# Optimization experiments

Hardware: AMD Instinct MI355X
Metric: run time of the kernel (lower is better)

## Reference

```python
import jax, jax.numpy as jnp
import numpy as np

B, N, E0, F_IN, H, EMB, VEC, DPI = 1024, 256, 2048, 6, 32, 32, 26, 512


def setup_inputs() -> dict:
    key = jax.random.key(0)
    ks = jax.random.split(key, 16)
    # fixed urban scene graph, shared by every batch element, with self-loops
    src0 = jax.random.randint(ks[0], (E0,), 0, N, dtype=jnp.int32)
    dst0 = jax.random.randint(ks[1], (E0,), 0, N, dtype=jnp.int32)
    loops = jnp.arange(N, dtype=jnp.int32)
    src = jnp.concatenate([src0, loops])
    dst = jnp.concatenate([dst0, loops])

    s = 0.05
    return {
        "graph_feats": jax.random.normal(ks[2], (B, N, F_IN), jnp.float32),
        "vector": jax.random.normal(ks[3], (B, VEC), jnp.float32),
        "src": src,
        "dst": dst,
        "W1": jax.random.normal(ks[4], (F_IN, H), jnp.float32) * s,
        "b1": jnp.zeros((H,), jnp.float32),
        "W2": jax.random.normal(ks[5], (H, H), jnp.float32) * s,
        "b2": jnp.zeros((H,), jnp.float32),
        "W3": jax.random.normal(ks[6], (H, H), jnp.float32) * s,
        "b3": jnp.zeros((H,), jnp.float32),
        "W_emb": jax.random.normal(ks[7], (H, EMB), jnp.float32) * s,
        "b_emb": jnp.zeros((EMB,), jnp.float32),
        "W_pi": jax.random.normal(ks[8], (VEC + EMB, DPI), jnp.float32) * s,
        "b_pi": jnp.zeros((DPI,), jnp.float32),
        "W_vf": jax.random.normal(ks[9], (VEC + EMB, DPI), jnp.float32) * s,
        "b_vf": jnp.zeros((DPI,), jnp.float32),
    }


def _edge_norm(src, dst, n_nodes):
    # DGL GraphConv norm='both': out_deg(src)^-1/2 * in_deg(dst)^-1/2
    ones = jnp.ones(src.shape[0], jnp.float32)
    deg_out = jax.ops.segment_sum(ones, src, num_segments=n_nodes)
    deg_in = jax.ops.segment_sum(ones, dst, num_segments=n_nodes)
    inv_o = jnp.where(deg_out > 0, deg_out ** -0.5, 0.0)
    inv_i = jnp.where(deg_in > 0, deg_in ** -0.5, 0.0)
    return inv_o[src] * inv_i[dst]  # [E]


def _gconv(h, src, dst, norm, W, b):
    # h: [B, N, F]; symmetric-normalized aggregation then linear (DGL GraphConv)
    msg = h[:, src, :] * norm[None, :, None]          # [B, E, F]
    agg = jnp.zeros_like(h).at[:, dst, :].add(msg)     # [B, N, F]
    return agg @ W + b


def reference(graph_feats, vector, src, dst, W1, b1, W2, b2, W3, b3,
              W_emb, b_emb, W_pi, b_pi, W_vf, b_vf):
    n_nodes = graph_feats.shape[1]
    norm = _edge_norm(src, dst, n_nodes)
    h = jax.nn.relu(_gconv(graph_feats, src, dst, norm, W1, b1))
    h = jax.nn.relu(_gconv(h, src, dst, norm, W2, b2))
    h = jax.nn.relu(_gconv(h, src, dst, norm, W3, b3))  # three_layers=True
    hg = jnp.mean(h, axis=1)                 # dgl.mean_nodes -> [B, H]
    emb = hg @ W_emb + b_emb                 # [B, EMB]
    comb = jnp.concatenate([vector[:, :26], emb], axis=1)  # [B, 58]
    pi = jax.nn.relu(comb @ W_pi + b_pi)
    vf = jax.nn.relu(comb @ W_vf + b_vf)
    return pi, vf
```

## Files before the change

### kernel.cpp

```cpp
#include <hip/hip_runtime.h>

#define B_    1024
#define N_    256
#define E_    2304
#define FIN_  6
#define VEC_  26
#define STR_  36

#define WS_ROWPTR   0
#define WS_PACKED   1088
#define WS_PERM     19520

__global__ __launch_bounds__(256) void prep_kernel(
    const int* __restrict__ src, const int* __restrict__ dst,
    char* __restrict__ ws)
{
    __shared__ int   deg_o[N_], deg_i[N_];
    __shared__ float inv_o[N_], inv_i[N_];
    __shared__ int   scan[N_];
    __shared__ int   rp[N_ + 1];
    __shared__ int   cursor[N_];
    __shared__ int   bcnt[64], boff[64];

    int*  row_ptr_g = (int*)(ws + WS_ROWPTR);
    int2* packed_g  = (int2*)(ws + WS_PACKED);
    int*  perm_g    = (int*)(ws + WS_PERM);

    const int t = threadIdx.x;

    deg_o[t] = 0; deg_i[t] = 0;
    if (t < 64) bcnt[t] = 0;
    __syncthreads();

    for (int e = t; e < E_; e += 256) {
        atomicAdd(&deg_o[src[e]], 1);
        atomicAdd(&deg_i[dst[e]], 1);
    }
    __syncthreads();
    {
        int dO = deg_o[t], dI = deg_i[t];
        inv_o[t] = dO > 0 ? rsqrtf((float)dO) : 0.f;
        inv_i[t] = dI > 0 ? rsqrtf((float)dI) : 0.f;
        scan[t] = dI;
    }
    __syncthreads();
    for (int off = 1; off < N_; off <<= 1) {
        int v = (t >= off) ? scan[t - off] : 0;
        __syncthreads();
        scan[t] += v;
        __syncthreads();
    }
    rp[t + 1] = scan[t];
    if (t == 0) rp[0] = 0;
    __syncthreads();
    cursor[t]    = rp[t];
    row_ptr_g[t] = rp[t];
    if (t == 0) row_ptr_g[N_] = rp[N_];
    __syncthreads();
    for (int e = t; e < E_; e += 256) {
        int d = dst[e], s = src[e];
        int pos = atomicAdd(&cursor[d], 1);
        packed_g[pos] = make_int2(s, __float_as_int(inv_o[s] * inv_i[d]));
    }

    int dmy = deg_i[t]; if (dmy > 63) dmy = 63;
    atomicAdd(&bcnt[dmy], 1);
    __syncthreads();
    if (t == 0) { int run = 0; for (int i = 0; i < 64; ++i) { boff[i] = run; run += bcnt[i]; } }
    __syncthreads();
    { int pos = atomicAdd(&boff[dmy], 1); perm_g[pos] = t; }
}

__global__ __launch_bounds__(256) void main_kernel(
    const float* __restrict__ gf,
    const float* __restrict__ vec,
    const float* __restrict__ W1, const float* __restrict__ b1,
    const float* __restrict__ W2, const float* __restrict__ b2,
    const float* __restrict__ W3, const float* __restrict__ b3,
    const float* __restrict__ We, const float* __restrict__ be,
    const float* __restrict__ Wpi, const float* __restrict__ bpi,
    const float* __restrict__ Wvf, const float* __restrict__ bvf,
    const char* __restrict__ ws,
    float2* __restrict__ out)
{
    __shared__ __align__(16) float buf[N_ * STR_];
    __shared__ float part[8 * 33];
    __shared__ float hgl[32];
    __shared__ float comb[VEC_ + 32];

    const int t = threadIdx.x;
    const int b = blockIdx.x;

    const int*  row_ptr = (const int*)(ws + WS_ROWPTR);
    const int2* packed  = (const int2*)(ws + WS_PACKED);
    const int   node    = ((const int*)(ws + WS_PERM))[t];

    {
        const float* g = gf + (size_t)b * (N_ * FIN_);
        for (int i = t; i < N_ * 8; i += 256) {
            int n = i >> 3, k = i & 7;
            buf[n * STR_ + k] = (k < FIN_) ? g[n * FIN_ + k] : 0.f;
        }
    }
    const int beg = row_ptr[node], end = row_ptr[node + 1];
    __syncthreads();

    float o[32];

    {
        float a[8] = {0,0,0,0,0,0,0,0};
        for (int e = beg; e < end; ++e) {
            int2 p = packed[e];
            float w = __int_as_float(p.y);
            const float4* hr = (const float4*)&buf[p.x * STR_];
            float4 c0 = hr[0], c1 = hr[1];
            a[0] += w * c0.x; a[1] += w * c0.y; a[2] += w * c0.z; a[3] += w * c0.w;
            a[4] += w * c1.x; a[5] += w * c1.y;
        }
#pragma unroll
        for (int j = 0; j < 32; ++j) o[j] = b1[j];
#pragma unroll
        for (int k = 0; k < FIN_; ++k) {
            float ak = a[k];
            const float* wr = &W1[k * 32];
#pragma unroll
            for (int j = 0; j < 32; ++j) o[j] += ak * wr[j];
        }
#pragma unroll
        for (int j = 0; j < 32; ++j) o[j] = fmaxf(o[j], 0.f);
    }
    __syncthreads();
    {
        float4* row = (float4*)&buf[node * STR_];
#pragma unroll
        for (int q = 0; q < 8; ++q) row[q] = make_float4(o[4*q], o[4*q+1], o[4*q+2], o[4*q+3]);
    }
    __syncthreads();

    for (int L = 0; L < 2; ++L) {
        float acc[32];
#pragma unroll
        for (int k = 0; k < 32; ++k) acc[k] = 0.f;
        for (int e = beg; e < end; ++e) {
            int2 p = packed[e];
            float w = __int_as_float(p.y);
            const float4* hr = (const float4*)&buf[p.x * STR_];
#pragma unroll
            for (int q = 0; q < 8; ++q) {
                float4 c = hr[q];
                acc[4*q]   += w * c.x;
                acc[4*q+1] += w * c.y;
                acc[4*q+2] += w * c.z;
                acc[4*q+3] += w * c.w;
            }
        }
        const float* Wl = (L == 0) ? W2 : W3;
        const float* Bl = (L == 0) ? b2 : b3;
#pragma unroll
        for (int j = 0; j < 32; ++j) o[j] = Bl[j];
#pragma unroll 8
        for (int k = 0; k < 32; ++k) {
            float ak = acc[k];
            const float* wr = &Wl[k * 32];
#pragma unroll
            for (int j = 0; j < 32; ++j) o[j] += ak * wr[j];
        }
#pragma unroll
        for (int j = 0; j < 32; ++j) o[j] = fmaxf(o[j], 0.f);
        __syncthreads();
        {
            float4* row = (float4*)&buf[node * STR_];
#pragma unroll
            for (int q = 0; q < 8; ++q) row[q] = make_float4(o[4*q], o[4*q+1], o[4*q+2], o[4*q+3]);
        }
        __syncthreads();
    }

    {
        int j = t & 31, g = t >> 5;
        float s = 0.f;
        for (int i = 0; i < 32; ++i) s += buf[(g * 32 + i) * STR_ + j];
        part[g * 33 + j] = s;
    }
    __syncthreads();
    if (t < 32) {
        float sum = 0.f;
#pragma unroll
        for (int g = 0; g < 8; ++g) sum += part[g * 33 + t];
        hgl[t] = sum * (1.0f / 256.0f);
    }
    __syncthreads();

    if (t < 32) {
        float v = be[t];
#pragma unroll
        for (int j = 0; j < 32; ++j) v += hgl[j] * We[j * 32 + t];
        comb[VEC_ + t] = v;
    }
    if (t < VEC_) comb[t] = vec[b * VEC_ + t];
    __syncthreads();

    {
        float p0 = bpi[2 * t], p1 = bpi[2 * t + 1];
        float v0 = bvf[2 * t], v1 = bvf[2 * t + 1];
        const float2* Wp = (const float2*)Wpi;
        const float2* Wv = (const float2*)Wvf;
        for (int k = 0; k < VEC_ + 32; ++k) {
            float c = comb[k];
            float2 a = Wp[k * 256 + t];
            p0 += c * a.x; p1 += c * a.y;
            float2 d = Wv[k * 256 + t];
            v0 += c * d.x; v1 += c * d.y;
        }
        out[b * 256 + t]          = make_float2(fmaxf(p0, 0.f), fmaxf(p1, 0.f));
        out[262144 + b * 256 + t] = make_float2(fmaxf(v0, 0.f), fmaxf(v1, 0.f));
    }
}

extern "C" void kernel_launch(void* const* d_in, const int* in_sizes, int n_in,
                              void* d_out, int out_size, void* d_ws, size_t ws_size,
                              hipStream_t stream)
{
    prep_kernel<<<1, 256, 0, stream>>>(
        (const int*)d_in[2], (const int*)d_in[3], (char*)d_ws);
    main_kernel<<<B_, 256, 0, stream>>>(
        (const float*)d_in[0], (const float*)d_in[1],
        (const float*)d_in[4], (const float*)d_in[5],
        (const float*)d_in[6], (const float*)d_in[7],
        (const float*)d_in[8], (const float*)d_in[9],
        (const float*)d_in[10], (const float*)d_in[11],
        (const float*)d_in[12], (const float*)d_in[13],
        (const float*)d_in[14], (const float*)d_in[15],
        (const char*)d_ws, (float2*)d_out);
}
```

Baseline: 138.4 us.

## Fuse graph CSR preprocessing into main kernel with fp16-packed edges in LDS

```diff
diff --git a/kernel.cpp b/kernel.cpp
--- a/kernel.cpp
+++ b/kernel.cpp
@@ -1,89 +1,28 @@
 #include <hip/hip_runtime.h>
+#include <hip/hip_fp16.h>
 
 #define B_    1024
 #define N_    256
 #define E_    2304
+#define EPT_  9
 #define FIN_  6
 #define VEC_  26
 #define STR_  36
 
-#define WS_ROWPTR   0
-#define WS_PACKED   1088
-#define WS_PERM     19520
-
-__global__ __launch_bounds__(256) void prep_kernel(
-    const int* __restrict__ src, const int* __restrict__ dst,
-    char* __restrict__ ws)
-{
-    __shared__ int   deg_o[N_], deg_i[N_];
-    __shared__ float inv_o[N_], inv_i[N_];
-    __shared__ int   scan[N_];
-    __shared__ int   rp[N_ + 1];
-    __shared__ int   cursor[N_];
-    __shared__ int   bcnt[64], boff[64];
-
-    int*  row_ptr_g = (int*)(ws + WS_ROWPTR);
-    int2* packed_g  = (int2*)(ws + WS_PACKED);
-    int*  perm_g    = (int*)(ws + WS_PERM);
-
-    const int t = threadIdx.x;
-
-    deg_o[t] = 0; deg_i[t] = 0;
-    if (t < 64) bcnt[t] = 0;
-    __syncthreads();
-
-    for (int e = t; e < E_; e += 256) {
-        atomicAdd(&deg_o[src[e]], 1);
-        atomicAdd(&deg_i[dst[e]], 1);
-    }
-    __syncthreads();
-    {
-        int dO = deg_o[t], dI = deg_i[t];
-        inv_o[t] = dO > 0 ? rsqrtf((float)dO) : 0.f;
-        inv_i[t] = dI > 0 ? rsqrtf((float)dI) : 0.f;
-        scan[t] = dI;
-    }
-    __syncthreads();
-    for (int off = 1; off < N_; off <<= 1) {
-        int v = (t >= off) ? scan[t - off] : 0;
-        __syncthreads();
-        scan[t] += v;
-        __syncthreads();
-    }
-    rp[t + 1] = scan[t];
-    if (t == 0) rp[0] = 0;
-    __syncthreads();
-    cursor[t]    = rp[t];
-    row_ptr_g[t] = rp[t];
-    if (t == 0) row_ptr_g[N_] = rp[N_];
-    __syncthreads();
-    for (int e = t; e < E_; e += 256) {
-        int d = dst[e], s = src[e];
-        int pos = atomicAdd(&cursor[d], 1);
-        packed_g[pos] = make_int2(s, __float_as_int(inv_o[s] * inv_i[d]));
-    }
-
-    int dmy = deg_i[t]; if (dmy > 63) dmy = 63;
-    atomicAdd(&bcnt[dmy], 1);
-    __syncthreads();
-    if (t == 0) { int run = 0; for (int i = 0; i < 64; ++i) { boff[i] = run; run += bcnt[i]; } }
-    __syncthreads();
-    { int pos = atomicAdd(&boff[dmy], 1); perm_g[pos] = t; }
-}
-
-__global__ __launch_bounds__(256) void main_kernel(
+__global__ __launch_bounds__(256) void fused_kernel(
     const float* __restrict__ gf,
     const float* __restrict__ vec,
+    const int* __restrict__ src, const int* __restrict__ dst,
     const float* __restrict__ W1, const float* __restrict__ b1,
     const float* __restrict__ W2, const float* __restrict__ b2,
     const float* __restrict__ W3, const float* __restrict__ b3,
     const float* __restrict__ We, const float* __restrict__ be,
     const float* __restrict__ Wpi, const float* __restrict__ bpi,
     const float* __restrict__ Wvf, const float* __restrict__ bvf,
-    const char* __restrict__ ws,
     float2* __restrict__ out)
 {
     __shared__ __align__(16) float buf[N_ * STR_];
+    __shared__ unsigned int packedE[E_];
     __shared__ float part[8 * 33];
     __shared__ float hgl[32];
     __shared__ float comb[VEC_ + 32];
@@ -91,9 +30,68 @@
     const int t = threadIdx.x;
     const int b = blockIdx.x;
 
-    const int*  row_ptr = (const int*)(ws + WS_ROWPTR);
-    const int2* packed  = (const int2*)(ws + WS_PACKED);
-    const int   node    = ((const int*)(ws + WS_PERM))[t];
+    int*   deg_o  = (int*)buf;
+    int*   deg_i  = (int*)buf + 256;
+    int*   scan   = (int*)buf + 512;
+    int*   cursor = (int*)buf + 768;
+    int*   bcnt   = (int*)buf + 1024;
+    int*   boff   = (int*)buf + 1088;
+    int*   perm   = (int*)buf + 1152;
+    float* inv_o  = buf + 1408;
+    float* inv_i  = buf + 1664;
+
+    deg_o[t] = 0; deg_i[t] = 0;
+    if (t < 64) bcnt[t] = 0;
+    __syncthreads();
+
+    int sB[EPT_], dB[EPT_];
+#pragma unroll
+    for (int i = 0; i < EPT_; ++i) {
+        int e = t + 256 * i;
+        sB[i] = src[e]; dB[i] = dst[e];
+    }
+#pragma unroll
+    for (int i = 0; i < EPT_; ++i) {
+        atomicAdd(&deg_o[sB[i]], 1);
+        atomicAdd(&deg_i[dB[i]], 1);
+    }
+    __syncthreads();
+
+    const int dI = deg_i[t];
+    {
+        int dO = deg_o[t];
+        inv_o[t] = dO > 0 ? rsqrtf((float)dO) : 0.f;
+        inv_i[t] = dI > 0 ? rsqrtf((float)dI) : 0.f;
+        scan[t] = dI;
+    }
+    __syncthreads();
+    for (int off = 1; off < N_; off <<= 1) {
+        int v = (t >= off) ? scan[t - off] : 0;
+        __syncthreads();
+        scan[t] += v;
+        __syncthreads();
+    }
+    cursor[t] = scan[t] - dI;
+    int dmy = dI > 63 ? 63 : dI;
+    atomicAdd(&bcnt[dmy], 1);
+    __syncthreads();
+    if (t == 0) { int run = 0; for (int i = 0; i < 64; ++i) { boff[i] = run; run += bcnt[i]; } }
+    __syncthreads();
+    { int pos = atomicAdd(&boff[dmy], 1); perm[pos] = t; }
+#pragma unroll
+    for (int i = 0; i < EPT_; ++i) {
+        int s = sB[i], d = dB[i];
+        int pos = atomicAdd(&cursor[d], 1);
+        float nrm = inv_o[s] * inv_i[d];
+        unsigned short h = __half_as_ushort(__float2half(nrm));
+        packedE[pos] = ((unsigned int)s << 16) | (unsigned int)h;
+    }
+    __syncthreads();
+
+    const int node = perm[t];
+    const int end  = scan[node];
+    const int beg  = end - deg_i[node];
+    __syncthreads();
 
     {
         const float* g = gf + (size_t)b * (N_ * FIN_);
@@ -102,7 +100,6 @@
             buf[n * STR_ + k] = (k < FIN_) ? g[n * FIN_ + k] : 0.f;
         }
     }
-    const int beg = row_ptr[node], end = row_ptr[node + 1];
     __syncthreads();
 
     float o[32];
@@ -110,9 +107,9 @@
     {
         float a[8] = {0,0,0,0,0,0,0,0};
         for (int e = beg; e < end; ++e) {
-            int2 p = packed[e];
-            float w = __int_as_float(p.y);
-            const float4* hr = (const float4*)&buf[p.x * STR_];
+            unsigned int u = packedE[e];
+            float w = __half2float(__ushort_as_half((unsigned short)(u & 0xffffu)));
+            const float4* hr = (const float4*)&buf[(u >> 16) * STR_];
             float4 c0 = hr[0], c1 = hr[1];
             a[0] += w * c0.x; a[1] += w * c0.y; a[2] += w * c0.z; a[3] += w * c0.w;
             a[4] += w * c1.x; a[5] += w * c1.y;
@@ -142,9 +139,9 @@
 #pragma unroll
         for (int k = 0; k < 32; ++k) acc[k] = 0.f;
         for (int e = beg; e < end; ++e) {
-            int2 p = packed[e];
-            float w = __int_as_float(p.y);
-            const float4* hr = (const float4*)&buf[p.x * STR_];
+            unsigned int u = packedE[e];
+            float w = __half2float(__ushort_as_half((unsigned short)(u & 0xffffu)));
+            const float4* hr = (const float4*)&buf[(u >> 16) * STR_];
 #pragma unroll
             for (int q = 0; q < 8; ++q) {
                 float4 c = hr[q];
@@ -221,15 +218,14 @@
                               void* d_out, int out_size, void* d_ws, size_t ws_size,
                               hipStream_t stream)
 {
-    prep_kernel<<<1, 256, 0, stream>>>(
-        (const int*)d_in[2], (const int*)d_in[3], (char*)d_ws);
-    main_kernel<<<B_, 256, 0, stream>>>(
+    fused_kernel<<<B_, 256, 0, stream>>>(
         (const float*)d_in[0], (const float*)d_in[1],
+        (const int*)d_in[2], (const int*)d_in[3],
         (const float*)d_in[4], (const float*)d_in[5],
         (const float*)d_in[6], (const float*)d_in[7],
         (const float*)d_in[8], (const float*)d_in[9],
         (const float*)d_in[10], (const float*)d_in[11],
         (const float*)d_in[12], (const float*)d_in[13],
         (const float*)d_in[14], (const float*)d_in[15],
-        (const char*)d_ws, (float2*)d_out);
+        (float2*)d_out);
 }
```

New measurement: 139.9 us. No clear change (+1.1%).

## Run GCN layers in packed fp16 with compressed edges staged in LDS

Applied to the files above, without the earlier changes.

```diff
diff --git a/kernel.cpp b/kernel.cpp
--- a/kernel.cpp
+++ b/kernel.cpp
@@ -1,18 +1,37 @@
 #include <hip/hip_runtime.h>
+#include <hip/hip_fp16.h>
 
 #define B_    1024
 #define N_    256
 #define E_    2304
 #define FIN_  6
 #define VEC_  26
-#define STR_  36
-
-#define WS_ROWPTR   0
-#define WS_PACKED   1088
-#define WS_PERM     19520
+#define HSTR_ 40
+
+#define WS_ROWPTR 0
+#define WS_PACKED 1088
+#define WS_PERM   10304
+#define WS_WH     11328
+#define OH_W1 0
+#define OH_W2 192
+#define OH_W3 1216
+#define OH_B1 2240
+#define OH_B2 2272
+#define OH_B3 2304
+
+__device__ __forceinline__ __half2 relu2(__half2 x) {
+    union { __half2 h; unsigned int u; } v;
+    v.h = x;
+    unsigned int mask = ((v.u & 0x80008000u) >> 15) * 0xFFFFu;
+    v.u &= ~mask;
+    return v.h;
+}
 
 __global__ __launch_bounds__(256) void prep_kernel(
     const int* __restrict__ src, const int* __restrict__ dst,
+    const float* __restrict__ W1, const float* __restrict__ b1,
+    const float* __restrict__ W2, const float* __restrict__ b2,
+    const float* __restrict__ W3, const float* __restrict__ b3,
     char* __restrict__ ws)
 {
     __shared__ int   deg_o[N_], deg_i[N_];
@@ -22,9 +41,10 @@
     __shared__ int   cursor[N_];
     __shared__ int   bcnt[64], boff[64];
 
-    int*  row_ptr_g = (int*)(ws + WS_ROWPTR);
-    int2* packed_g  = (int2*)(ws + WS_PACKED);
-    int*  perm_g    = (int*)(ws + WS_PERM);
+    int*          row_ptr_g = (int*)(ws + WS_ROWPTR);
+    unsigned int* packed_g  = (unsigned int*)(ws + WS_PACKED);
+    int*          perm_g    = (int*)(ws + WS_PERM);
+    __half*       Wh        = (__half*)(ws + WS_WH);
 
     const int t = threadIdx.x;
 
@@ -60,7 +80,9 @@
     for (int e = t; e < E_; e += 256) {
         int d = dst[e], s = src[e];
         int pos = atomicAdd(&cursor[d], 1);
-        packed_g[pos] = make_int2(s, __float_as_int(inv_o[s] * inv_i[d]));
+        float nrm = inv_o[s] * inv_i[d];
+        unsigned short h = __half_as_ushort(__float2half(nrm));
+        packed_g[pos] = ((unsigned int)s << 16) | (unsigned int)h;
     }
 
     int dmy = deg_i[t]; if (dmy > 63) dmy = 63;
@@ -69,21 +91,28 @@
     if (t == 0) { int run = 0; for (int i = 0; i < 64; ++i) { boff[i] = run; run += bcnt[i]; } }
     __syncthreads();
     { int pos = atomicAdd(&boff[dmy], 1); perm_g[pos] = t; }
+
+    for (int i = t; i < 192;  i += 256) Wh[OH_W1 + i] = __float2half(W1[i]);
+    for (int i = t; i < 1024; i += 256) Wh[OH_W2 + i] = __float2half(W2[i]);
+    for (int i = t; i < 1024; i += 256) Wh[OH_W3 + i] = __float2half(W3[i]);
+    if (t < 32) {
+        Wh[OH_B1 + t] = __float2half(b1[t]);
+        Wh[OH_B2 + t] = __float2half(b2[t]);
+        Wh[OH_B3 + t] = __float2half(b3[t]);
+    }
 }
 
 __global__ __launch_bounds__(256) void main_kernel(
     const float* __restrict__ gf,
     const float* __restrict__ vec,
-    const float* __restrict__ W1, const float* __restrict__ b1,
-    const float* __restrict__ W2, const float* __restrict__ b2,
-    const float* __restrict__ W3, const float* __restrict__ b3,
     const float* __restrict__ We, const float* __restrict__ be,
     const float* __restrict__ Wpi, const float* __restrict__ bpi,
     const float* __restrict__ Wvf, const float* __restrict__ bvf,
     const char* __restrict__ ws,
     float2* __restrict__ out)
 {
-    __shared__ __align__(16) float buf[N_ * STR_];
+    __shared__ __align__(16) __half hbuf[N_ * HSTR_];
+    __shared__ unsigned int packedE[E_];
     __shared__ float part[8 * 33];
     __shared__ float hgl[32];
     __shared__ float comb[VEC_ + 32];
@@ -91,102 +120,122 @@
     const int t = threadIdx.x;
     const int b = blockIdx.x;
 
-    const int*  row_ptr = (const int*)(ws + WS_ROWPTR);
-    const int2* packed  = (const int2*)(ws + WS_PACKED);
-    const int   node    = ((const int*)(ws + WS_PERM))[t];
+    const int*          row_ptr = (const int*)(ws + WS_ROWPTR);
+    const unsigned int* packedG = (const unsigned int*)(ws + WS_PACKED);
+    const int           node    = ((const int*)(ws + WS_PERM))[t];
+    const __half*       Wh      = (const __half*)(ws + WS_WH);
+
+    const int beg = row_ptr[node], end = row_ptr[node + 1];
+
+    for (int e = t; e < E_; e += 256) packedE[e] = packedG[e];
 
     {
         const float* g = gf + (size_t)b * (N_ * FIN_);
         for (int i = t; i < N_ * 8; i += 256) {
             int n = i >> 3, k = i & 7;
-            buf[n * STR_ + k] = (k < FIN_) ? g[n * FIN_ + k] : 0.f;
-        }
-    }
-    const int beg = row_ptr[node], end = row_ptr[node + 1];
-    __syncthreads();
-
-    float o[32];
-
-    {
-        float a[8] = {0,0,0,0,0,0,0,0};
+            hbuf[n * HSTR_ + k] = __float2half((k < FIN_) ? g[n * FIN_ + k] : 0.f);
+        }
+    }
+    __syncthreads();
+
+    const __half2 z2 = __float2half2_rn(0.f);
+    __half2 o2[16];
+
+    {
+        __half2 a2[4] = {z2, z2, z2, z2};
         for (int e = beg; e < end; ++e) {
-            int2 p = packed[e];
-            float w = __int_as_float(p.y);
-            const float4* hr = (const float4*)&buf[p.x * STR_];
-            float4 c0 = hr[0], c1 = hr[1];
-            a[0] += w * c0.x; a[1] += w * c0.y; a[2] += w * c0.z; a[3] += w * c0.w;
-            a[4] += w * c1.x; a[5] += w * c1.y;
-        }
-#pragma unroll
-        for (int j = 0; j < 32; ++j) o[j] = b1[j];
+            unsigned int u = packedE[e];
+            __half2 w2 = __half2half2(__ushort_as_half((unsigned short)(u & 0xffffu)));
+            union { float4 f4; __half2 h2[4]; } r;
+            r.f4 = *(const float4*)&hbuf[(u >> 16) * HSTR_];
+#pragma unroll
+            for (int q = 0; q < 4; ++q) a2[q] = __hfma2(w2, r.h2[q], a2[q]);
+        }
+        const __half2* bh = (const __half2*)(Wh + OH_B1);
+#pragma unroll
+        for (int j = 0; j < 16; ++j) o2[j] = bh[j];
 #pragma unroll
         for (int k = 0; k < FIN_; ++k) {
-            float ak = a[k];
-            const float* wr = &W1[k * 32];
-#pragma unroll
-            for (int j = 0; j < 32; ++j) o[j] += ak * wr[j];
-        }
-#pragma unroll
-        for (int j = 0; j < 32; ++j) o[j] = fmaxf(o[j], 0.f);
-    }
-    __syncthreads();
-    {
-        float4* row = (float4*)&buf[node * STR_];
-#pragma unroll
-        for (int q = 0; q < 8; ++q) row[q] = make_float4(o[4*q], o[4*q+1], o[4*q+2], o[4*q+3]);
+            __half ak = (k & 1) ? __high2half(a2[k >> 1]) : __low2half(a2[k >> 1]);
+            __half2 ak2 = __half2half2(ak);
+            const __half2* wr = (const __half2*)(Wh + OH_W1 + k * 32);
+#pragma unroll
+            for (int j = 0; j < 16; ++j) o2[j] = __hfma2(ak2, wr[j], o2[j]);
+        }
+#pragma unroll
+        for (int j = 0; j < 16; ++j) o2[j] = relu2(o2[j]);
+    }
+    __syncthreads();
+    {
+        union { float4 f4; __half2 h2[4]; } w;
+        float4* row = (float4*)&hbuf[node * HSTR_];
+#pragma unroll
+        for (int q = 0; q < 4; ++q) {
+#pragma unroll
+            for (int r = 0; r < 4; ++r) w.h2[r] = o2[4 * q + r];
+            row[q] = w.f4;
+        }
     }
     __syncthreads();
 
     for (int L = 0; L < 2; ++L) {
-        float acc[32];
-#pragma unroll
-        for (int k = 0; k < 32; ++k) acc[k] = 0.f;
+        __half2 acc2[16];
+#pragma unroll
+        for (int j = 0; j < 16; ++j) acc2[j] = z2;
         for (int e = beg; e < end; ++e) {
-            int2 p = packed[e];
-            float w = __int_as_float(p.y);
-            const float4* hr = (const float4*)&buf[p.x * STR_];
-#pragma unroll
-            for (int q = 0; q < 8; ++q) {
-                float4 c = hr[q];
-                acc[4*q]   += w * c.x;
-                acc[4*q+1] += w * c.y;
-                acc[4*q+2] += w * c.z;
-                acc[4*q+3] += w * c.w;
+            unsigned int u = packedE[e];
+            __half2 w2 = __half2half2(__ushort_as_half((unsigned short)(u & 0xffffu)));
+            const float4* hr = (const float4*)&hbuf[(u >> 16) * HSTR_];
+            union { float4 f4; __half2 h2[4]; } r0, r1, r2, r3;
+            r0.f4 = hr[0]; r1.f4 = hr[1]; r2.f4 = hr[2]; r3.f4 = hr[3];
+#pragma unroll
+            for (int q = 0; q < 4; ++q) {
+                acc2[q]      = __hfma2(w2, r0.h2[q], acc2[q]);
+                acc2[4 + q]  = __hfma2(w2, r1.h2[q], acc2[4 + q]);
+                acc2[8 + q]  = __hfma2(w2, r2.h2[q], acc2[8 + q]);
+                acc2[12 + q] = __hfma2(w2, r3.h2[q], acc2[12 + q]);
             }
         }
-        const float* Wl = (L == 0) ? W2 : W3;
-        const float* Bl = (L == 0) ? b2 : b3;
-#pragma unroll
-        for (int j = 0; j < 32; ++j) o[j] = Bl[j];
+        const __half*  Whl = Wh + (L == 0 ? OH_W2 : OH_W3);
+        const __half2* bh  = (const __half2*)(Wh + (L == 0 ? OH_B2 : OH_B3));
+#pragma unroll
+        for (int j = 0; j < 16; ++j) o2[j] = bh[j];
 #pragma unroll 8
         for (int k = 0; k < 32; ++k) {
-            float ak = acc[k];
-            const float* wr = &Wl[k * 32];
-#pragma unroll
-            for (int j = 0; j < 32; ++j) o[j] += ak * wr[j];
-        }
-#pragma unroll
-        for (int j = 0; j < 32; ++j) o[j] = fmaxf(o[j], 0.f);
+            __half ak = (k & 1) ? __high2half(acc2[k >> 1]) : __low2half(acc2[k >> 1]);
+            __half2 ak2 = __half2half2(ak);
+            const __half2* wr = (const __half2*)(Whl + k * 32);
+#pragma unroll
+            for (int j = 0; j < 16; ++j) o2[j] = __hfma2(ak2, wr[j], o2[j]);
+        }
+#pragma unroll
+        for (int j = 0; j < 16; ++j) o2[j] = relu2(o2[j]);
         __syncthreads();
         {
-            float4* row = (float4*)&buf[node * STR_];
-#pragma unroll
-            for (int q = 0; q < 8; ++q) row[q] = make_float4(o[4*q], o[4*q+1], o[4*q+2], o[4*q+3]);
-        }
-        __syncthreads();
-    }
-
-    {
-        int j = t & 31, g = t >> 5;
+            union { float4 f4; __half2 h2[4]; } w;
+            float4* row = (float4*)&hbuf[node * HSTR_];
+#pragma unroll
+            for (int q = 0; q < 4; ++q) {
+#pragma unroll
+                for (int r = 0; r < 4; ++r) w.h2[r] = o2[4 * q + r];
+                row[q] = w.f4;
+            }
+        }
+        __syncthreads();
+    }
+
+    {
+        int j = t & 31, g8 = t >> 5;
         float s = 0.f;
-        for (int i = 0; i < 32; ++i) s += buf[(g * 32 + i) * STR_ + j];
-        part[g * 33 + j] = s;
+        for (int i = 0; i < 32; ++i)
+            s += __half2float(hbuf[(g8 * 32 + i) * HSTR_ + j]);
+        part[g8 * 33 + j] = s;
     }
     __syncthreads();
     if (t < 32) {
         float sum = 0.f;
 #pragma unroll
-        for (int g = 0; g < 8; ++g) sum += part[g * 33 + t];
+        for (int g8 = 0; g8 < 8; ++g8) sum += part[g8 * 33 + t];
         hgl[t] = sum * (1.0f / 256.0f);
     }
     __syncthreads();
@@ -222,12 +271,13 @@
                               hipStream_t stream)
 {
     prep_kernel<<<1, 256, 0, stream>>>(
-        (const int*)d_in[2], (const int*)d_in[3], (char*)d_ws);
-    main_kernel<<<B_, 256, 0, stream>>>(
-        (const float*)d_in[0], (const float*)d_in[1],
+        (const int*)d_in[2], (const int*)d_in[3],
         (const float*)d_in[4], (const float*)d_in[5],
         (const float*)d_in[6], (const float*)d_in[7],
         (const float*)d_in[8], (const float*)d_in[9],
+        (char*)d_ws);
+    main_kernel<<<B_, 256, 0, stream>>>(
+        (const float*)d_in[0], (const float*)d_in[1],
         (const float*)d_in[10], (const float*)d_in[11],
         (const float*)d_in[12], (const float*)d_in[13],
         (const float*)d_in[14], (const float*)d_in[15],
```

New measurement: 138.3 us. Within noise of the previous version (-0.1%).

## Replace sparse gather aggregation with dense fp16 adjacency MFMA matmuls

Applied to the files above, without the earlier changes.

```diff
diff --git a/kernel.cpp b/kernel.cpp
--- a/kernel.cpp
+++ b/kernel.cpp
@@ -1,37 +1,33 @@
 #include <hip/hip_runtime.h>
+#include <hip/hip_fp16.h>
 
 #define B_    1024
 #define N_    256
 #define E_    2304
 #define FIN_  6
 #define VEC_  26
-#define STR_  36
-
-#define WS_ROWPTR   0
-#define WS_PACKED   1088
-#define WS_PERM     19520
+#define HSTR_ 40
+#define ZSTR_ 264
+#define NT_   512
+
+typedef _Float16 half8 __attribute__((ext_vector_type(8)));
+typedef float    f32x4 __attribute__((ext_vector_type(4)));
+
 
 __global__ __launch_bounds__(256) void prep_kernel(
     const int* __restrict__ src, const int* __restrict__ dst,
     char* __restrict__ ws)
 {
-    __shared__ int   deg_o[N_], deg_i[N_];
+    __shared__ int   deg_o[N_], deg_i[N_], scan[N_], rp[N_ + 1], cursor[N_];
     __shared__ float inv_o[N_], inv_i[N_];
-    __shared__ int   scan[N_];
-    __shared__ int   rp[N_ + 1];
-    __shared__ int   cursor[N_];
-    __shared__ int   bcnt[64], boff[64];
-
-    int*  row_ptr_g = (int*)(ws + WS_ROWPTR);
-    int2* packed_g  = (int2*)(ws + WS_PACKED);
-    int*  perm_g    = (int*)(ws + WS_PERM);
+    __shared__ unsigned int packedE[E_];
 
     const int t = threadIdx.x;
+    __half*       A   = (__half*)ws;
+    unsigned int* A32 = (unsigned int*)ws;
 
     deg_o[t] = 0; deg_i[t] = 0;
-    if (t < 64) bcnt[t] = 0;
-    __syncthreads();
-
+    __syncthreads();
     for (int e = t; e < E_; e += 256) {
         atomicAdd(&deg_o[src[e]], 1);
         atomicAdd(&deg_i[dst[e]], 1);
@@ -53,25 +49,27 @@
     rp[t + 1] = scan[t];
     if (t == 0) rp[0] = 0;
     __syncthreads();
-    cursor[t]    = rp[t];
-    row_ptr_g[t] = rp[t];
-    if (t == 0) row_ptr_g[N_] = rp[N_];
+    cursor[t] = rp[t];
     __syncthreads();
     for (int e = t; e < E_; e += 256) {
         int d = dst[e], s = src[e];
         int pos = atomicAdd(&cursor[d], 1);
-        packed_g[pos] = make_int2(s, __float_as_int(inv_o[s] * inv_i[d]));
-    }
-
-    int dmy = deg_i[t]; if (dmy > 63) dmy = 63;
-    atomicAdd(&bcnt[dmy], 1);
-    __syncthreads();
-    if (t == 0) { int run = 0; for (int i = 0; i < 64; ++i) { boff[i] = run; run += bcnt[i]; } }
-    __syncthreads();
-    { int pos = atomicAdd(&boff[dmy], 1); perm_g[pos] = t; }
+        float nrm = inv_o[s] * inv_i[d];
+        packedE[pos] = ((unsigned int)s << 16)
+                     | (unsigned int)__half_as_ushort(__float2half(nrm));
+    }
+    for (int i = t; i < 32768; i += 256) A32[i] = 0u;
+    __syncthreads();
+    for (int e = rp[t]; e < rp[t + 1]; ++e) {
+        unsigned int u = packedE[e];
+        int s = (int)(u >> 16);
+        float nv = __half2float(__ushort_as_half((unsigned short)(u & 0xffffu)));
+        __half* p = &A[t * 256 + s];
+        *p = __float2half(__half2float(*p) + nv);
+    }
 }
 
-__global__ __launch_bounds__(256) void main_kernel(
+__global__ __launch_bounds__(512) void main_kernel(
     const float* __restrict__ gf,
     const float* __restrict__ vec,
     const float* __restrict__ W1, const float* __restrict__ b1,
@@ -81,112 +79,136 @@
     const float* __restrict__ Wpi, const float* __restrict__ bpi,
     const float* __restrict__ Wvf, const float* __restrict__ bvf,
     const char* __restrict__ ws,
-    float2* __restrict__ out)
+    float* __restrict__ out)
 {
-    __shared__ __align__(16) float buf[N_ * STR_];
-    __shared__ float part[8 * 33];
+    __shared__ __align__(16) __half hbuf[N_ * HSTR_];
+    __shared__ __align__(16) __half zT[32 * ZSTR_];
+    __shared__ float part[16 * 33];
     __shared__ float hgl[32];
     __shared__ float comb[VEC_ + 32];
 
     const int t = threadIdx.x;
     const int b = blockIdx.x;
-
-    const int*  row_ptr = (const int*)(ws + WS_ROWPTR);
-    const int2* packed  = (const int2*)(ws + WS_PACKED);
-    const int   node    = ((const int*)(ws + WS_PERM))[t];
-
-    {
-        const float* g = gf + (size_t)b * (N_ * FIN_);
-        for (int i = t; i < N_ * 8; i += 256) {
-            int n = i >> 3, k = i & 7;
-            buf[n * STR_ + k] = (k < FIN_) ? g[n * FIN_ + k] : 0.f;
-        }
-    }
-    const int beg = row_ptr[node], end = row_ptr[node + 1];
-    __syncthreads();
-
-    float o[32];
-
-    {
-        float a[8] = {0,0,0,0,0,0,0,0};
-        for (int e = beg; e < end; ++e) {
-            int2 p = packed[e];
-            float w = __int_as_float(p.y);
-            const float4* hr = (const float4*)&buf[p.x * STR_];
-            float4 c0 = hr[0], c1 = hr[1];
-            a[0] += w * c0.x; a[1] += w * c0.y; a[2] += w * c0.z; a[3] += w * c0.w;
-            a[4] += w * c1.x; a[5] += w * c1.y;
-        }
-#pragma unroll
-        for (int j = 0; j < 32; ++j) o[j] = b1[j];
-#pragma unroll
-        for (int k = 0; k < FIN_; ++k) {
-            float ak = a[k];
-            const float* wr = &W1[k * 32];
-#pragma unroll
-            for (int j = 0; j < 32; ++j) o[j] += ak * wr[j];
-        }
-#pragma unroll
-        for (int j = 0; j < 32; ++j) o[j] = fmaxf(o[j], 0.f);
-    }
-    __syncthreads();
-    {
-        float4* row = (float4*)&buf[node * STR_];
-#pragma unroll
-        for (int q = 0; q < 8; ++q) row[q] = make_float4(o[4*q], o[4*q+1], o[4*q+2], o[4*q+3]);
-    }
-    __syncthreads();
-
-    for (int L = 0; L < 2; ++L) {
-        float acc[32];
-#pragma unroll
-        for (int k = 0; k < 32; ++k) acc[k] = 0.f;
-        for (int e = beg; e < end; ++e) {
-            int2 p = packed[e];
-            float w = __int_as_float(p.y);
-            const float4* hr = (const float4*)&buf[p.x * STR_];
-#pragma unroll
-            for (int q = 0; q < 8; ++q) {
-                float4 c = hr[q];
-                acc[4*q]   += w * c.x;
-                acc[4*q+1] += w * c.y;
-                acc[4*q+2] += w * c.z;
-                acc[4*q+3] += w * c.w;
-            }
-        }
-        const float* Wl = (L == 0) ? W2 : W3;
-        const float* Bl = (L == 0) ? b2 : b3;
-#pragma unroll
-        for (int j = 0; j < 32; ++j) o[j] = Bl[j];
-#pragma unroll 8
-        for (int k = 0; k < 32; ++k) {
-            float ak = acc[k];
-            const float* wr = &Wl[k * 32];
-#pragma unroll
-            for (int j = 0; j < 32; ++j) o[j] += ak * wr[j];
-        }
-#pragma unroll
-        for (int j = 0; j < 32; ++j) o[j] = fmaxf(o[j], 0.f);
+    const int lane = t & 63, wv = t >> 6, sub = t & 1;
+    const int node = t >> 1;
+    const int m16 = lane & 15, q4 = lane >> 4;
+    const int slab = wv * 32;
+    const __half* A = (const __half*)ws;
+
+    {
+        const float* x0 = gf + (size_t)b * (N_ * FIN_) + node * FIN_;
+        float xr[FIN_];
+#pragma unroll
+        for (int c = 0; c < FIN_; ++c) xr[c] = x0[c];
+        const int j0 = sub * 16;
+        float o[16];
+#pragma unroll
+        for (int j = 0; j < 16; ++j) o[j] = 0.f;
+#pragma unroll
+        for (int c = 0; c < FIN_; ++c) {
+            float xc = xr[c];
+            const float* wr = &W1[c * 32 + j0];
+#pragma unroll
+            for (int j = 0; j < 16; ++j) o[j] += xc * wr[j];
+        }
+#pragma unroll
+        for (int j = 0; j < 16; ++j)
+            zT[(j0 + j) * ZSTR_ + node] = __float2half(o[j]);
+    }
+    __syncthreads();
+
+    for (int L = 0; L < 3; ++L) {
+        const float* Bl = (L == 0) ? b1 : (L == 1) ? b2 : b3;
+
+        if (L > 0) {
+            const float* Wl = (L == 1) ? W2 : W3;
+            half8 af[2], bf[2];
+#pragma unroll
+            for (int g = 0; g < 2; ++g) {
+                union { float4 f4; half8 h8; } u;
+                u.f4 = *(const float4*)&hbuf[(slab + g * 16 + m16) * HSTR_ + q4 * 8];
+                af[g] = u.h8;
+            }
+#pragma unroll
+            for (int h = 0; h < 2; ++h) {
+#pragma unroll
+                for (int j = 0; j < 8; ++j)
+                    bf[h][j] = (_Float16)Wl[(q4 * 8 + j) * 32 + h * 16 + m16];
+            }
+            f32x4 Z[2][2];
+#pragma unroll
+            for (int g = 0; g < 2; ++g) {
+#pragma unroll
+                for (int h = 0; h < 2; ++h) {
+                    f32x4 zz = {0.f, 0.f, 0.f, 0.f};
+                    Z[g][h] = __builtin_amdgcn_mfma_f32_16x16x32_f16(af[g], bf[h], zz, 0, 0, 0);
+                }
+            }
+#pragma unroll
+            for (int g = 0; g < 2; ++g)
+#pragma unroll
+                for (int h = 0; h < 2; ++h)
+#pragma unroll
+                    for (int r = 0; r < 4; ++r)
+                        zT[(h * 16 + m16) * ZSTR_ + slab + g * 16 + q4 * 4 + r]
+                            = __float2half(Z[g][h][r]);
+            __syncthreads();
+        }
+
+        {
+            f32x4 D[2][2];
+#pragma unroll
+            for (int g = 0; g < 2; ++g)
+#pragma unroll
+                for (int h = 0; h < 2; ++h) {
+                    float bc = Bl[h * 16 + m16];
+                    f32x4 c = {bc, bc, bc, bc};
+                    D[g][h] = c;
+                }
+            for (int kk = 0; kk < 8; ++kk) {
+                half8 af[2], bf[2];
+#pragma unroll
+                for (int g = 0; g < 2; ++g) {
+                    union { float4 f4; half8 h8; } u;
+                    u.f4 = *(const float4*)&A[(slab + g * 16 + m16) * 256 + kk * 32 + q4 * 8];
+                    af[g] = u.h8;
+                }
+#pragma unroll
+                for (int h = 0; h < 2; ++h) {
+                    union { float4 f4; half8 h8; } u;
+                    u.f4 = *(const float4*)&zT[(h * 16 + m16) * ZSTR_ + kk * 32 + q4 * 8];
+                    bf[h] = u.h8;
+                }
+#pragma unroll
+                for (int g = 0; g < 2; ++g)
+#pragma unroll
+                    for (int h = 0; h < 2; ++h)
+                        D[g][h] = __builtin_amdgcn_mfma_f32_16x16x32_f16(af[g], bf[h], D[g][h], 0, 0, 0);
+            }
+#pragma unroll
+            for (int g = 0; g < 2; ++g)
+#pragma unroll
+                for (int h = 0; h < 2; ++h)
+#pragma unroll
+                    for (int r = 0; r < 4; ++r)
+                        hbuf[(slab + g * 16 + q4 * 4 + r) * HSTR_ + h * 16 + m16]
+                            = __float2half(fmaxf(D[g][h][r], 0.f));
+        }
         __syncthreads();
-        {
-            float4* row = (float4*)&buf[node * STR_];
-#pragma unroll
-            for (int q = 0; q < 8; ++q) row[q] = make_float4(o[4*q], o[4*q+1], o[4*q+2], o[4*q+3]);
-        }
-        __syncthreads();
-    }
-
-    {
-        int j = t & 31, g = t >> 5;
+    }
+
+    {
+        int j = t & 31, g16 = t >> 5;
         float s = 0.f;
-        for (int i = 0; i < 32; ++i) s += buf[(g * 32 + i) * STR_ + j];
-        part[g * 33 + j] = s;
+        for (int i = 0; i < 16; ++i)
+            s += __half2float(hbuf[(g16 * 16 + i) * HSTR_ + j]);
+        part[g16 * 33 + j] = s;
     }
     __syncthreads();
     if (t < 32) {
         float sum = 0.f;
 #pragma unroll
-        for (int g = 0; g < 8; ++g) sum += part[g * 33 + t];
+        for (int g16 = 0; g16 < 16; ++g16) sum += part[g16 * 33 + t];
         hgl[t] = sum * (1.0f / 256.0f);
     }
     __syncthreads();
@@ -201,19 +223,14 @@
     __syncthreads();
 
     {
-        float p0 = bpi[2 * t], p1 = bpi[2 * t + 1];
-        float v0 = bvf[2 * t], v1 = bvf[2 * t + 1];
-        const float2* Wp = (const float2*)Wpi;
-        const float2* Wv = (const float2*)Wvf;
+        float p = bpi[t], v = bvf[t];
         for (int k = 0; k < VEC_ + 32; ++k) {
             float c = comb[k];
-            float2 a = Wp[k * 256 + t];
-            p0 += c * a.x; p1 += c * a.y;
-            float2 d = Wv[k * 256 + t];
-            v0 += c * d.x; v1 += c * d.y;
-        }
-        out[b * 256 + t]          = make_float2(fmaxf(p0, 0.f), fmaxf(p1, 0.f));
-        out[262144 + b * 256 + t] = make_float2(fmaxf(v0, 0.f), fmaxf(v1, 0.f));
+            p += c * Wpi[k * 512 + t];
+            v += c * Wvf[k * 512 + t];
+        }
+        out[(size_t)b * 512 + t]          = fmaxf(p, 0.f);
+        out[524288 + (size_t)b * 512 + t] = fmaxf(v, 0.f);
     }
 }
 
@@ -223,7 +240,7 @@
 {
     prep_kernel<<<1, 256, 0, stream>>>(
         (const int*)d_in[2], (const int*)d_in[3], (char*)d_ws);
-    main_kernel<<<B_, 256, 0, stream>>>(
+    main_kernel<<<B_, NT_, 0, stream>>>(
         (const float*)d_in[0], (const float*)d_in[1],
         (const float*)d_in[4], (const float*)d_in[5],
         (const float*)d_in[6], (const float*)d_in[7],
@@ -231,5 +248,5 @@
         (const float*)d_in[10], (const float*)d_in[11],
         (const float*)d_in[12], (const float*)d_in[13],
         (const float*)d_in[14], (const float*)d_in[15],
-        (const char*)d_ws, (float2*)d_out);
+        (const char*)d_ws, (float*)d_out);
 }
```

Result: slower. 152.6 us (+10.3%).
